# Optimization experiments

Hardware: AMD Instinct MI355X
Metric: run time of the kernel (lower is better)

Reference implementation:

```python
import jax, jax.numpy as jnp
import numpy as np
from jax import lax

N, T, V, E, H, D, B = 16384, 16, 10000, 256, 256, 512, 128


def setup_inputs() -> dict:
    key = jax.random.key(0)
    ks = jax.random.split(key, 12)
    tok = jax.random.randint(ks[0], (N, T), 1, V)
    lens = jax.random.randint(ks[1], (N,), 4, T + 1)
    tok = jnp.where(jnp.arange(T)[None, :] < lens[:, None], tok, 0)  # pad_id = 0
    ast_path_len = jnp.full((B,), N // B, dtype=jnp.int32)  # 128 paths per sample
    u = lambda k, s: jax.random.uniform(k, s, jnp.float32, -0.1, 0.1)
    emb = u(ks[2], (V, E)).at[0].set(0.0)  # padding_idx=0 row zeroed
    return {
        "ast_path": tok,
        "ast_path_len": ast_path_len,
        "emb": emb,
        "W_ih_f": u(ks[3], (4 * H, E)), "W_hh_f": u(ks[4], (4 * H, H)), "b_f": u(ks[5], (4 * H,)),
        "W_ih_b": u(ks[6], (4 * H, E)), "W_hh_b": u(ks[7], (4 * H, H)), "b_b": u(ks[8], (4 * H,)),
        "W_lin": u(ks[9], (D, 2 * H)), "b_lin": jnp.zeros((D,), jnp.float32),
    }


def _lstm_final_h(x_tm, lens, W_ih, W_hh, b, reverse):
    # x_tm: [T, N, E]; returns final hidden state [N, H] honoring per-seq length
    n = x_tm.shape[1]
    h0 = jnp.zeros((n, H), x_tm.dtype)

    def step(carry, xt):
        h, c = carry
        x, t = xt
        gates = x @ W_ih.T + h @ W_hh.T + b  # [N, 4H]
        i, f, g, o = jnp.split(gates, 4, axis=-1)
        c_new = jax.nn.sigmoid(f) * c + jax.nn.sigmoid(i) * jnp.tanh(g)
        h_new = jax.nn.sigmoid(o) * jnp.tanh(c_new)
        m = (t < lens)[:, None]  # packed-sequence semantics: frozen past length
        return (jnp.where(m, h_new, h), jnp.where(m, c_new, c)), None

    (h, _), _ = lax.scan(step, (h0, h0), (x_tm, jnp.arange(x_tm.shape[0])), reverse=reverse)
    return h


def reference(ast_path, ast_path_len, emb, W_ih_f, W_hh_f, b_f, W_ih_b, W_hh_b, b_b, W_lin, b_lin):
    lens = (ast_path != 0).sum(axis=-1)  # pad_id = 0
    x = emb[ast_path]                     # [N, T, E]; dropout is identity at eval
    x_tm = jnp.swapaxes(x, 0, 1)          # [T, N, E]
    h_fwd = _lstm_final_h(x_tm, lens, W_ih_f, W_hh_f, b_f, reverse=False)
    h_bwd = _lstm_final_h(x_tm, lens, W_ih_b, W_hh_b, b_b, reverse=True)
    h_n = jnp.concatenate([h_fwd, h_bwd], axis=1)        # [N, 2H]
    repr_ = h_n @ W_lin.T + b_lin                         # [N, D]
    # segment-mean pooling over path groups (replaces the Python loop)
    n_paths = repr_.shape[0]
    seg_ids = jnp.repeat(jnp.arange(ast_path_len.shape[0]), ast_path_len,
                         total_repeat_length=n_paths)
    sums = jax.ops.segment_sum(repr_, seg_ids, num_segments=ast_path_len.shape[0])
    pooled = sums / ast_path_len[:, None].astype(repr_.dtype)  # [B, D]
    norm = jnp.sqrt(jnp.sum(pooled * pooled, axis=-1, keepdims=True))
    return pooled / jnp.maximum(norm, 1e-5)
```

## Files before the change

### kernel.cpp

```cpp
#include <hip/hip_runtime.h>
#include <stdint.h>

#define N_SEQ 16384
#define T_LEN 16
#define E_DIM 256
#define H_DIM 256
#define K_DIM 512
#define B_SAMP 128
#define V_SIZE 10000

typedef __bf16 bf16x8 __attribute__((ext_vector_type(8)));
typedef float  f32x4  __attribute__((ext_vector_type(4)));
typedef unsigned short ush;

__device__ __forceinline__ ush f2bf(float x) {
  unsigned int u = __float_as_uint(x);
  u = (u + 0x7fffu + ((u >> 16) & 1u)) >> 16;
  return (ush)u;
}
__device__ __forceinline__ float bf2f(ush v) {
  return __uint_as_float(((unsigned int)v) << 16);
}
__device__ __forceinline__ float sigmoidf_(float x) {
  return 1.0f / (1.0f + __expf(-x));
}
__device__ __forceinline__ float tanhf_(float x) {
  float e = __expf(2.0f * x);
  return 1.0f - 2.0f / (e + 1.0f);
}
__device__ __forceinline__ void glds16(const void* g, const void* l) {
  __builtin_amdgcn_global_load_lds(
      (const __attribute__((address_space(1))) unsigned int*)g,
      (__attribute__((address_space(3))) unsigned int*)l, 16, 0, 0);
}


__global__ __launch_bounds__(256) void k_lens(const int* __restrict__ tok, int* __restrict__ lens,
                                              int* __restrict__ hist) {
  __shared__ int lh[17];
  if (threadIdx.x < 17) lh[threadIdx.x] = 0;
  __syncthreads();
  int n = blockIdx.x * 256 + threadIdx.x;
  const int* r = tok + n * T_LEN;
  int c = 0;
#pragma unroll
  for (int t = 0; t < T_LEN; ++t) c += (r[t] != 0);
  lens[n] = c;
  atomicAdd(&lh[c], 1);
  __syncthreads();
  if (threadIdx.x < 17 && lh[threadIdx.x]) atomicAdd(&hist[threadIdx.x], lh[threadIdx.x]);
}

__global__ void k_offsets(const int* __restrict__ hist, int* __restrict__ cursor,
                          int* __restrict__ cnts_f, int* __restrict__ cnts_b) {
  if (threadIdx.x == 0) {
    int off = 0;
    for (int l = 16; l >= 0; --l) { cursor[l] = off; off += hist[l]; }
    for (int t = 0; t < 16; ++t) {
      int cf = 0, cb = 0;
      for (int l = t; l <= 16; ++l) cf += hist[l];
      for (int l = t + 1; l <= 16; ++l) cb += hist[l];
      cnts_f[t] = cf;
      cnts_b[t] = cb;
    }
  }
}

__global__ __launch_bounds__(256) void k_scatter(const int* __restrict__ lens, int* __restrict__ cursor,
                                                 int* __restrict__ perm, int* __restrict__ pinv,
                                                 int* __restrict__ plens) {
  int n = blockIdx.x * 256 + threadIdx.x;
  int l = lens[n];
  int pos = atomicAdd(&cursor[l], 1);
  perm[pos] = n;
  pinv[n] = pos;
  plens[pos] = l;
}

__global__ __launch_bounds__(256) void k_tokperm(const int* __restrict__ tok, const int* __restrict__ perm,
                                                 int* __restrict__ tokperm) {
  int id = blockIdx.x * 256 + threadIdx.x;
  int t = id >> 14;
  int pos = id & (N_SEQ - 1);
  tokperm[id] = tok[perm[pos] * T_LEN + t];
}

__global__ __launch_bounds__(256) void k_embcvt(const float* __restrict__ emb, ush* __restrict__ out) {
  int i = blockIdx.x * 256 + threadIdx.x;
  out[i] = f2bf(emb[i]);
}

__global__ __launch_bounds__(256) void k_wprep(const float* __restrict__ Wih_f, const float* __restrict__ Whh_f,
                                               const float* __restrict__ Wih_b, const float* __restrict__ Whh_b,
                                               ush* __restrict__ wpt_f, ush* __restrict__ wpt_b) {
  int id = blockIdx.x * 256 + threadIdx.x;
  int dir = id >> 19;
  int rem = id & ((1 << 19) - 1);
  int p = rem >> 9;
  int k = rem & 511;
  int nb = p >> 8, wc = (p >> 6) & 3, q = (p >> 4) & 3, jj = p & 15;
  int r = q * 256 + nb * 64 + wc * 16 + jj;
  const float* Wih = dir ? Wih_b : Wih_f;
  const float* Whh = dir ? Whh_b : Whh_f;
  float v = (k < 256) ? Wih[r * 256 + k] : Whh[r * 256 + (k - 256)];
  ush* o = dir ? wpt_b : wpt_f;
  o[p * 512 + k] = f2bf(v);
}


__global__ __launch_bounds__(512, 4)
void k_step(const ush* __restrict__ embbf, const int* __restrict__ tokperm,
            const int* __restrict__ plens,
            const int* __restrict__ cnts_f, const int* __restrict__ cnts_b,
            const ush* __restrict__ wpt_f, const ush* __restrict__ wpt_b,
            const float* __restrict__ bias_f, const float* __restrict__ bias_b,
            const ush* __restrict__ hr_f, ush* __restrict__ hw_f,
            const ush* __restrict__ hr_b, ush* __restrict__ hw_b,
            ush* __restrict__ cT_f, ush* __restrict__ cT_b,
            int s) {
  const int dir = blockIdx.y;
  const int t = dir ? (15 - s) : s;
  const int cnt = dir ? cnts_b[t] : cnts_f[t];
  const int mblk = blockIdx.x >> 2;
  const int m0 = mblk * 128;
  if (m0 >= cnt) return;

  const int nblk = blockIdx.x & 3;
  const ush* wpt = dir ? wpt_b : wpt_f;
  const float* bias = dir ? bias_b : bias_f;
  const ush* hr = dir ? hr_b : hr_f;
  ush* hw = dir ? hw_b : hw_f;
  ush* cT = dir ? cT_b : cT_f;

  __shared__ __align__(128) unsigned char ldsA[128 * 128];
  __shared__ __align__(128) unsigned char ldsB[256 * 128];

  const int tid = threadIdx.x;
  const int lane = tid & 63;
  const int w = tid >> 6;
  const int wr = w >> 2;
  const int wc = w & 3;
  const int frow = lane & 15;
  const int fkq = lane >> 4;

  const int j = nblk * 64 + wc * 16 + frow;
  const float b0 = bias[j], b1 = bias[256 + j], b2 = bias[512 + j], b3 = bias[768 + j];
  int4 l4[4];
  ushort4 cvu[4];
#pragma unroll
  for (int fr = 0; fr < 4; ++fr) {
    const int n0 = m0 + wr * 64 + fr * 16 + fkq * 4;
    l4[fr] = *(const int4*)&plens[n0];
    cvu[fr] = *(const ushort4*)&cT[(size_t)j * N_SEQ + n0];
  }

  const int l8 = lane >> 3;
  const int l7 = lane & 7;
  const int arow0 = 16 * w + l8;
  const int arow1 = arow0 + 8;
  const int ach0 = l7 ^ (arow0 & 7);
  const int ach1 = l7 ^ (arow1 & 7);
  const unsigned aoffE0 = (unsigned)tokperm[t * N_SEQ + m0 + arow0] * E_DIM + ach0 * 8;
  const unsigned aoffE1 = (unsigned)tokperm[t * N_SEQ + m0 + arow1] * E_DIM + ach1 * 8;
  const unsigned aoffH0 = (unsigned)(m0 + arow0) * H_DIM + ach0 * 8;
  const unsigned aoffH1 = (unsigned)(m0 + arow1) * H_DIM + ach1 * 8;
  unsigned boff[4];
#pragma unroll
  for (int jj = 0; jj < 4; ++jj) {
    const int brow = 32 * w + 8 * jj + l8;
    const int bch = l7 ^ (brow & 7);
    boff[jj] = (unsigned)(nblk * 256 + brow) * K_DIM + bch * 8;
  }

  f32x4 acc[4][4] = {};

  for (int kt = 0; kt < 8; ++kt) {
    const int k0 = kt * 64;
    if (kt < 4) {
      glds16(embbf + aoffE0 + k0, &ldsA[(16 * w) * 128]);
      glds16(embbf + aoffE1 + k0, &ldsA[(16 * w + 8) * 128]);
    } else {
      glds16(hr + aoffH0 + (k0 - E_DIM), &ldsA[(16 * w) * 128]);
      glds16(hr + aoffH1 + (k0 - E_DIM), &ldsA[(16 * w + 8) * 128]);
    }
#pragma unroll
    for (int jj = 0; jj < 4; ++jj)
      glds16(wpt + boff[jj] + k0, &ldsB[(32 * w + 8 * jj) * 128]);
    __syncthreads();
#pragma unroll
    for (int ksub = 0; ksub < 2; ++ksub) {
      bf16x8 av[4], bv[4];
#pragma unroll
      for (int fr = 0; fr < 4; ++fr) {
        const int row = wr * 64 + fr * 16 + frow;
        const int ch = (ksub * 4 + fkq) ^ (row & 7);
        av[fr] = *(const bf16x8*)&ldsA[row * 128 + ch * 16];
      }
#pragma unroll
      for (int fc = 0; fc < 4; ++fc) {
        const int row = wc * 64 + fc * 16 + frow;
        const int ch = (ksub * 4 + fkq) ^ (row & 7);
        bv[fc] = *(const bf16x8*)&ldsB[row * 128 + ch * 16];
      }
      __builtin_amdgcn_s_setprio(1);
#pragma unroll
      for (int fr = 0; fr < 4; ++fr)
#pragma unroll
        for (int fc = 0; fc < 4; ++fc)
          acc[fr][fc] = __builtin_amdgcn_mfma_f32_16x16x32_bf16(av[fr], bv[fc], acc[fr][fc], 0, 0, 0);
      __builtin_amdgcn_s_setprio(0);
    }
    __syncthreads();
  }

#pragma unroll
  for (int fr = 0; fr < 4; ++fr) {
    const int n0 = m0 + wr * 64 + fr * 16 + fkq * 4;
    const int4 ln = l4[fr];
    const int lmax = max(max(ln.x, ln.y), max(ln.z, ln.w));
    float cv[4] = {bf2f(cvu[fr].x), bf2f(cvu[fr].y), bf2f(cvu[fr].z), bf2f(cvu[fr].w)};
    const f32x4 gi = acc[fr][0], gf = acc[fr][1], gg = acc[fr][2], go = acc[fr][3];
#pragma unroll
    for (int r = 0; r < 4; ++r) {
      const int lnv = (r == 0) ? ln.x : (r == 1) ? ln.y : (r == 2) ? ln.z : ln.w;
      const size_t hidx = (size_t)(n0 + r) * H_DIM + j;
      if (t < lnv) {
        const float iv = sigmoidf_(gi[r] + b0);
        const float fv = sigmoidf_(gf[r] + b1);
        const float gv = tanhf_(gg[r] + b2);
        const float ov = sigmoidf_(go[r] + b3);
        const bool first = dir ? (t == lnv - 1) : (t == 0);
        const float cn = fv * (first ? 0.0f : cv[r]) + iv * gv;
        cv[r] = cn;
        hw[hidx] = f2bf(ov * tanhf_(cn));
      } else if (!dir) {
        hw[hidx] = hr[hidx];
      }
    }
    if (t < lmax) {
      ushort4 cu = make_ushort4(f2bf(cv[0]), f2bf(cv[1]), f2bf(cv[2]), f2bf(cv[3]));
      *(ushort4*)&cT[(size_t)j * N_SEQ + n0] = cu;
    }
  }
}


__global__ __launch_bounds__(256) void k_pool(const ush* __restrict__ hf,
                                              const ush* __restrict__ hb,
                                              const int* __restrict__ pinv,
                                              const int* __restrict__ plen,
                                              float* __restrict__ pooled) {
  const int b = blockIdx.x, tid = threadIdx.x;
  int start = 0;
  for (int i = 0; i < b; ++i) start += plen[i];
  const int cnt = plen[b];
  float s0 = 0.f, s1 = 0.f;
  for (int r = 0; r < cnt; ++r) {
    const size_t pr = (size_t)pinv[start + r];
    s0 += bf2f(hf[pr * H_DIM + tid]);
    s1 += bf2f(hb[pr * H_DIM + tid]);
  }
  float inv = 1.0f / (float)cnt;
  pooled[b * 512 + tid] = s0 * inv;
  pooled[b * 512 + H_DIM + tid] = s1 * inv;
}


__global__ __launch_bounds__(256) void k_final(const float* __restrict__ pooled,
                                               const float* __restrict__ W,
                                               const float* __restrict__ bl,
                                               float* __restrict__ out) {
  const int b = blockIdx.x, tid = threadIdx.x;
  __shared__ float pv[512];
  __shared__ float pre[512];
  __shared__ float red[4];
  pv[tid] = pooled[b * 512 + tid];
  pv[tid + 256] = pooled[b * 512 + 256 + tid];
  __syncthreads();
#pragma unroll
  for (int half = 0; half < 2; ++half) {
    const int dd = tid + half * 256;
    const f32x4* wr = (const f32x4*)(W + (size_t)dd * 512);
    const f32x4* pvv = (const f32x4*)pv;
    float s = bl[dd];
#pragma unroll 4
    for (int k4 = 0; k4 < 128; ++k4) {
      f32x4 wv = wr[k4], xv = pvv[k4];
      s += wv[0] * xv[0] + wv[1] * xv[1] + wv[2] * xv[2] + wv[3] * xv[3];
    }
    pre[dd] = s;
  }
  __syncthreads();
  float ss = pre[tid] * pre[tid] + pre[tid + 256] * pre[tid + 256];
#pragma unroll
  for (int off = 32; off > 0; off >>= 1) ss += __shfl_down(ss, off, 64);
  if ((tid & 63) == 0) red[tid >> 6] = ss;
  __syncthreads();
  float tot = red[0] + red[1] + red[2] + red[3];
  float scale = 1.0f / fmaxf(sqrtf(tot), 1e-5f);
  out[b * 512 + tid] = pre[tid] * scale;
  out[b * 512 + 256 + tid] = pre[tid + 256] * scale;
}


extern "C" void kernel_launch(void* const* d_in, const int* in_sizes, int n_in,
                              void* d_out, int out_size, void* d_ws, size_t ws_size,
                              hipStream_t stream) {
  const int* tok    = (const int*)d_in[0];
  const int* plen   = (const int*)d_in[1];
  const float* emb  = (const float*)d_in[2];
  const float* Wih_f = (const float*)d_in[3];
  const float* Whh_f = (const float*)d_in[4];
  const float* b_f   = (const float*)d_in[5];
  const float* Wih_b = (const float*)d_in[6];
  const float* Whh_b = (const float*)d_in[7];
  const float* b_b   = (const float*)d_in[8];
  const float* Wlin  = (const float*)d_in[9];
  const float* blin  = (const float*)d_in[10];
  float* out = (float*)d_out;

  char* ws = (char*)d_ws;
  size_t off = 0;
  auto alloc = [&](size_t bytes) {
    void* p = ws + off;
    off = (off + bytes + 255) & ~(size_t)255;
    return p;
  };
  ush* embbf   = (ush*)alloc((size_t)V_SIZE * E_DIM * 2);
  ush* wptf    = (ush*)alloc((size_t)1024 * K_DIM * 2);
  ush* wptb    = (ush*)alloc((size_t)1024 * K_DIM * 2);
  int* lens    = (int*)alloc((size_t)N_SEQ * 4);
  int* perm    = (int*)alloc((size_t)N_SEQ * 4);
  int* pinv    = (int*)alloc((size_t)N_SEQ * 4);
  int* plens   = (int*)alloc((size_t)N_SEQ * 4);
  int* tokperm = (int*)alloc((size_t)T_LEN * N_SEQ * 4);
  int* hist    = (int*)alloc(17 * 4);
  int* cursor  = (int*)alloc(17 * 4);
  int* cntsf   = (int*)alloc(16 * 4);
  int* cntsb   = (int*)alloc(16 * 4);
  ush* h0f     = (ush*)alloc((size_t)N_SEQ * H_DIM * 2);
  ush* h1f     = (ush*)alloc((size_t)N_SEQ * H_DIM * 2);
  ush* h0b     = (ush*)alloc((size_t)N_SEQ * H_DIM * 2);
  ush* h1b     = (ush*)alloc((size_t)N_SEQ * H_DIM * 2);
  ush* cTf     = (ush*)alloc((size_t)H_DIM * N_SEQ * 2);
  ush* cTb     = (ush*)alloc((size_t)H_DIM * N_SEQ * 2);
  float* pooled = (float*)alloc((size_t)B_SAMP * 512 * 4);

  hipMemsetAsync(hist, 0, 17 * 4, stream);
  hipMemsetAsync(h0f, 0, (size_t)N_SEQ * H_DIM * 2, stream);
  hipMemsetAsync(h1f, 0, (size_t)N_SEQ * H_DIM * 2, stream);
  hipMemsetAsync(h0b, 0, (size_t)N_SEQ * H_DIM * 2, stream);
  hipMemsetAsync(h1b, 0, (size_t)N_SEQ * H_DIM * 2, stream);

  k_lens<<<N_SEQ / 256, 256, 0, stream>>>(tok, lens, hist);
  k_offsets<<<1, 64, 0, stream>>>(hist, cursor, cntsf, cntsb);
  k_scatter<<<N_SEQ / 256, 256, 0, stream>>>(lens, cursor, perm, pinv, plens);
  k_tokperm<<<(T_LEN * N_SEQ) / 256, 256, 0, stream>>>(tok, perm, tokperm);
  k_embcvt<<<(V_SIZE * E_DIM) / 256, 256, 0, stream>>>(emb, embbf);
  k_wprep<<<(2 * 1024 * K_DIM) / 256, 256, 0, stream>>>(Wih_f, Whh_f, Wih_b, Whh_b, wptf, wptb);

  dim3 grid(512, 2);
  for (int s = 0; s < T_LEN; ++s) {
    const ush* hrf = (s & 1) ? h1f : h0f;
    ush* hwf       = (s & 1) ? h0f : h1f;
    const ush* hrb = (s & 1) ? h1b : h0b;
    ush* hwb       = (s & 1) ? h0b : h1b;
    k_step<<<grid, 512, 0, stream>>>(embbf, tokperm, plens, cntsf, cntsb, wptf, wptb,
                                     b_f, b_b, hrf, hwf, hrb, hwb, cTf, cTb, s);
  }
  k_pool<<<B_SAMP, 256, 0, stream>>>(h0f, h0b, pinv, plen, pooled);
  k_final<<<B_SAMP, 256, 0, stream>>>(pooled, Wlin, blin, out);
}
```

Before: 990.4 us.

## Drop forward h copy for finished rows and keep cell state in fp32

The forward direction no longer copies the previous hidden state for sequences past their length. Instead, the pooling kernel picks the ping-pong buffer that holds each sequence's final state, using the parity of its length. The cell state moves from a transposed bf16 buffer to a row-major fp32 buffer that is read and written per element only for active rows, and a single active-count table now serves both directions. The s_setprio hints around the MFMA loop are removed. This cuts h copy traffic and avoids bf16 rounding of c, at the cost of wider, less vectorised cell-state accesses.

```diff
diff --git a/kernel.cpp b/kernel.cpp
--- a/kernel.cpp
+++ b/kernel.cpp
@@ -52,16 +52,14 @@
 }
 
 __global__ void k_offsets(const int* __restrict__ hist, int* __restrict__ cursor,
-                          int* __restrict__ cnts_f, int* __restrict__ cnts_b) {
+                          int* __restrict__ cnts) {
   if (threadIdx.x == 0) {
     int off = 0;
     for (int l = 16; l >= 0; --l) { cursor[l] = off; off += hist[l]; }
     for (int t = 0; t < 16; ++t) {
-      int cf = 0, cb = 0;
-      for (int l = t; l <= 16; ++l) cf += hist[l];
-      for (int l = t + 1; l <= 16; ++l) cb += hist[l];
-      cnts_f[t] = cf;
-      cnts_b[t] = cb;
+      int c = 0;
+      for (int l = t + 1; l <= 16; ++l) c += hist[l];
+      cnts[t] = c;
     }
   }
 }
@@ -110,17 +108,16 @@
 
 __global__ __launch_bounds__(512, 4)
 void k_step(const ush* __restrict__ embbf, const int* __restrict__ tokperm,
-            const int* __restrict__ plens,
-            const int* __restrict__ cnts_f, const int* __restrict__ cnts_b,
+            const int* __restrict__ plens, const int* __restrict__ cnts,
             const ush* __restrict__ wpt_f, const ush* __restrict__ wpt_b,
             const float* __restrict__ bias_f, const float* __restrict__ bias_b,
             const ush* __restrict__ hr_f, ush* __restrict__ hw_f,
             const ush* __restrict__ hr_b, ush* __restrict__ hw_b,
-            ush* __restrict__ cT_f, ush* __restrict__ cT_b,
+            float* __restrict__ c_f, float* __restrict__ c_b,
             int s) {
   const int dir = blockIdx.y;
   const int t = dir ? (15 - s) : s;
-  const int cnt = dir ? cnts_b[t] : cnts_f[t];
+  const int cnt = cnts[t];
   const int mblk = blockIdx.x >> 2;
   const int m0 = mblk * 128;
   if (m0 >= cnt) return;
@@ -130,7 +127,7 @@
   const float* bias = dir ? bias_b : bias_f;
   const ush* hr = dir ? hr_b : hr_f;
   ush* hw = dir ? hw_b : hw_f;
-  ush* cT = dir ? cT_b : cT_f;
+  float* cc = dir ? c_b : c_f;
 
   __shared__ __align__(128) unsigned char ldsA[128 * 128];
   __shared__ __align__(128) unsigned char ldsB[256 * 128];
@@ -140,19 +137,6 @@
   const int w = tid >> 6;
   const int wr = w >> 2;
   const int wc = w & 3;
-  const int frow = lane & 15;
-  const int fkq = lane >> 4;
-
-  const int j = nblk * 64 + wc * 16 + frow;
-  const float b0 = bias[j], b1 = bias[256 + j], b2 = bias[512 + j], b3 = bias[768 + j];
-  int4 l4[4];
-  ushort4 cvu[4];
-#pragma unroll
-  for (int fr = 0; fr < 4; ++fr) {
-    const int n0 = m0 + wr * 64 + fr * 16 + fkq * 4;
-    l4[fr] = *(const int4*)&plens[n0];
-    cvu[fr] = *(const ushort4*)&cT[(size_t)j * N_SEQ + n0];
-  }
 
   const int l8 = lane >> 3;
   const int l7 = lane & 7;
@@ -173,6 +157,8 @@
   }
 
   f32x4 acc[4][4] = {};
+  const int frow = lane & 15;
+  const int fkq = lane >> 4;
 
   for (int kt = 0; kt < 8; ++kt) {
     const int k0 = kt * 64;
@@ -202,52 +188,44 @@
         const int ch = (ksub * 4 + fkq) ^ (row & 7);
         bv[fc] = *(const bf16x8*)&ldsB[row * 128 + ch * 16];
       }
-      __builtin_amdgcn_s_setprio(1);
 #pragma unroll
       for (int fr = 0; fr < 4; ++fr)
 #pragma unroll
         for (int fc = 0; fc < 4; ++fc)
           acc[fr][fc] = __builtin_amdgcn_mfma_f32_16x16x32_bf16(av[fr], bv[fc], acc[fr][fc], 0, 0, 0);
-      __builtin_amdgcn_s_setprio(0);
     }
     __syncthreads();
   }
 
+  const int j = nblk * 64 + wc * 16 + frow;
+  const float b0 = bias[j], b1 = bias[256 + j], b2 = bias[512 + j], b3 = bias[768 + j];
 #pragma unroll
   for (int fr = 0; fr < 4; ++fr) {
     const int n0 = m0 + wr * 64 + fr * 16 + fkq * 4;
-    const int4 ln = l4[fr];
-    const int lmax = max(max(ln.x, ln.y), max(ln.z, ln.w));
-    float cv[4] = {bf2f(cvu[fr].x), bf2f(cvu[fr].y), bf2f(cvu[fr].z), bf2f(cvu[fr].w)};
+    const int4 l4 = *(const int4*)&plens[n0];
     const f32x4 gi = acc[fr][0], gf = acc[fr][1], gg = acc[fr][2], go = acc[fr][3];
 #pragma unroll
     for (int r = 0; r < 4; ++r) {
-      const int lnv = (r == 0) ? ln.x : (r == 1) ? ln.y : (r == 2) ? ln.z : ln.w;
-      const size_t hidx = (size_t)(n0 + r) * H_DIM + j;
+      const int lnv = (r == 0) ? l4.x : (r == 1) ? l4.y : (r == 2) ? l4.z : l4.w;
       if (t < lnv) {
+        const size_t idx = (size_t)(n0 + r) * H_DIM + j;
         const float iv = sigmoidf_(gi[r] + b0);
         const float fv = sigmoidf_(gf[r] + b1);
         const float gv = tanhf_(gg[r] + b2);
         const float ov = sigmoidf_(go[r] + b3);
         const bool first = dir ? (t == lnv - 1) : (t == 0);
-        const float cn = fv * (first ? 0.0f : cv[r]) + iv * gv;
-        cv[r] = cn;
-        hw[hidx] = f2bf(ov * tanhf_(cn));
-      } else if (!dir) {
-        hw[hidx] = hr[hidx];
+        const float cn = fv * (first ? 0.0f : cc[idx]) + iv * gv;
+        cc[idx] = cn;
+        hw[idx] = f2bf(ov * tanhf_(cn));
       }
     }
-    if (t < lmax) {
-      ushort4 cu = make_ushort4(f2bf(cv[0]), f2bf(cv[1]), f2bf(cv[2]), f2bf(cv[3]));
-      *(ushort4*)&cT[(size_t)j * N_SEQ + n0] = cu;
-    }
-  }
-}
-
-
-__global__ __launch_bounds__(256) void k_pool(const ush* __restrict__ hf,
-                                              const ush* __restrict__ hb,
-                                              const int* __restrict__ pinv,
+  }
+}
+
+
+__global__ __launch_bounds__(256) void k_pool(const ush* __restrict__ h0f, const ush* __restrict__ h1f,
+                                              const ush* __restrict__ h0b,
+                                              const int* __restrict__ pinv, const int* __restrict__ lens,
                                               const int* __restrict__ plen,
                                               float* __restrict__ pooled) {
   const int b = blockIdx.x, tid = threadIdx.x;
@@ -256,9 +234,12 @@
   const int cnt = plen[b];
   float s0 = 0.f, s1 = 0.f;
   for (int r = 0; r < cnt; ++r) {
-    const size_t pr = (size_t)pinv[start + r];
+    const int n = start + r;
+    const size_t pr = (size_t)pinv[n];
+    const int l = lens[n];
+    const ush* hf = (l & 1) ? h1f : h0f;
     s0 += bf2f(hf[pr * H_DIM + tid]);
-    s1 += bf2f(hb[pr * H_DIM + tid]);
+    s1 += bf2f(h0b[pr * H_DIM + tid]);
   }
   float inv = 1.0f / (float)cnt;
   pooled[b * 512 + tid] = s0 * inv;
@@ -336,14 +317,13 @@
   int* tokperm = (int*)alloc((size_t)T_LEN * N_SEQ * 4);
   int* hist    = (int*)alloc(17 * 4);
   int* cursor  = (int*)alloc(17 * 4);
-  int* cntsf   = (int*)alloc(16 * 4);
-  int* cntsb   = (int*)alloc(16 * 4);
+  int* cnts    = (int*)alloc(16 * 4);
   ush* h0f     = (ush*)alloc((size_t)N_SEQ * H_DIM * 2);
   ush* h1f     = (ush*)alloc((size_t)N_SEQ * H_DIM * 2);
   ush* h0b     = (ush*)alloc((size_t)N_SEQ * H_DIM * 2);
   ush* h1b     = (ush*)alloc((size_t)N_SEQ * H_DIM * 2);
-  ush* cTf     = (ush*)alloc((size_t)H_DIM * N_SEQ * 2);
-  ush* cTb     = (ush*)alloc((size_t)H_DIM * N_SEQ * 2);
+  float* cf    = (float*)alloc((size_t)N_SEQ * H_DIM * 4);
+  float* cb    = (float*)alloc((size_t)N_SEQ * H_DIM * 4);
   float* pooled = (float*)alloc((size_t)B_SAMP * 512 * 4);
 
   hipMemsetAsync(hist, 0, 17 * 4, stream);
@@ -353,7 +333,7 @@
   hipMemsetAsync(h1b, 0, (size_t)N_SEQ * H_DIM * 2, stream);
 
   k_lens<<<N_SEQ / 256, 256, 0, stream>>>(tok, lens, hist);
-  k_offsets<<<1, 64, 0, stream>>>(hist, cursor, cntsf, cntsb);
+  k_offsets<<<1, 64, 0, stream>>>(hist, cursor, cnts);
   k_scatter<<<N_SEQ / 256, 256, 0, stream>>>(lens, cursor, perm, pinv, plens);
   k_tokperm<<<(T_LEN * N_SEQ) / 256, 256, 0, stream>>>(tok, perm, tokperm);
   k_embcvt<<<(V_SIZE * E_DIM) / 256, 256, 0, stream>>>(emb, embbf);
@@ -365,9 +345,9 @@
     ush* hwf       = (s & 1) ? h0f : h1f;
     const ush* hrb = (s & 1) ? h1b : h0b;
     ush* hwb       = (s & 1) ? h0b : h1b;
-    k_step<<<grid, 512, 0, stream>>>(embbf, tokperm, plens, cntsf, cntsb, wptf, wptb,
-                                     b_f, b_b, hrf, hwf, hrb, hwb, cTf, cTb, s);
-  }
-  k_pool<<<B_SAMP, 256, 0, stream>>>(h0f, h0b, pinv, plen, pooled);
+    k_step<<<grid, 512, 0, stream>>>(embbf, tokperm, plens, cnts, wptf, wptb,
+                                     b_f, b_b, hrf, hwf, hrb, hwb, cf, cb, s);
+  }
+  k_pool<<<B_SAMP, 256, 0, stream>>>(h0f, h1f, h0b, pinv, lens, plen, pooled);
   k_final<<<B_SAMP, 256, 0, stream>>>(pooled, Wlin, blin, out);
 }
```

Measured after the change: 845.2 us. -14.7%, faster.
